# Optimization experiments

Hardware: AMD Instinct MI355X
Metric: run time of the kernel (lower is better)

The kernel has to match this reference:

```python
import jax, jax.numpy as jnp
import numpy as np

SCORE_THR = 0.005   # score_thres is None in init -> default 0.005
IOU_THR = 0.5
TOPK = 1024         # fixed pre-NMS candidate cap (JAX needs static shapes)


def setup_inputs() -> dict:
    key = jax.random.key(0)
    # (B, 4+nc, N_anchors): 16 images, 80 classes, 33600 anchors (1280x1280, strides 8/16/32)
    x = jax.random.normal(key, (16, 84, 33600), dtype=jnp.float32)
    return {"x": x}


def _pairwise_iou(b):
    # b: (K, 4) xyxy. Same math as torchvision.ops.box_iou.
    lt = jnp.maximum(b[:, None, :2], b[None, :, :2])   # (K, K, 2)
    rb = jnp.minimum(b[:, None, 2:], b[None, :, 2:])   # (K, K, 2)
    wh = jnp.clip(rb - lt, 0.0)
    inter = wh[..., 0] * wh[..., 1]
    area = (b[:, 2] - b[:, 0]) * (b[:, 3] - b[:, 1])
    union = area[:, None] + area[None, :] - inter
    return inter / jnp.maximum(union, 1e-9)


def _nms_single(boxes, svals, cids):
    # boxes (N,4); svals (N,) with -inf where score <= threshold; cids (N,) int
    top_s, idx = jax.lax.top_k(svals, TOPK)            # score-descending candidates
    b = boxes[idx]                                      # (K, 4)
    c = cids[idx]                                       # (K,)
    valid = top_s > SCORE_THR                           # thresholded-out slots are -inf
    iou = _pairwise_iou(b)                              # (K, K)
    ar = jnp.arange(TOPK)

    def body(i, keep):
        # greedy NMS: box i (if still kept) suppresses lower-scored boxes with IoU > thr
        sup = (iou[i] > IOU_THR) & (ar > i) & keep[i]
        return keep & ~sup

    keep = jax.lax.fori_loop(0, TOPK, body, valid)
    out = jnp.concatenate([b, top_s[:, None], c[:, None].astype(jnp.float32)], axis=1)  # (K, 6)
    out = jnp.where(keep[:, None], out, 0.0)            # padded fixed-size result
    return out, keep


def reference(x):
    xt = jnp.transpose(x, (0, 2, 1))                    # (B, N, 4+nc)
    boxes, scores = xt[..., :4], xt[..., 4:]
    svals = scores.max(-1)                              # (B, N)
    cids = scores.argmax(-1)                            # (B, N)
    svals = jnp.where(svals > SCORE_THR, svals, -jnp.inf)  # score-threshold mask
    out, keep = jax.vmap(_nms_single)(boxes, svals, cids)
    # out: (B, TOPK, 6) zero-padded [xyxy, score, cls]; keep: (B, TOPK) validity mask
    return out, keep
```

## Files before the change

### kernel.cpp

```cpp
#include <hip/hip_runtime.h>
#include <cstdint>
#include <cstddef>

#define NB 16
#define NC 84
#define NA 33600
#define NCLS 80
#define TOPK 1024
#define NBIN 8192
#define CANDCAP 8192
#define SELCAP 2048
#define SCORE_THR 0.005f
#define IOU_THR 0.5f
#define SBLK 33
#define SORTT 1024

__device__ __forceinline__ unsigned mono_u32(float f) {
    unsigned u = __float_as_uint(f);
    return (u & 0x80000000u) ? ~u : (u | 0x80000000u);
}
__device__ __forceinline__ float key_val(uint64_t k) {
    unsigned u = (unsigned)(k >> 32);
    u = (u & 0x80000000u) ? (u & 0x7FFFFFFFu) : ~u;
    return __uint_as_float(u);
}
__device__ __forceinline__ int key_idx(uint64_t k) {
    return (int)(~(uint32_t)(k & 0xFFFFFFFFu));
}

__global__ __launch_bounds__(256) void score_hist_kernel(const float* __restrict__ x,
                                                         float* __restrict__ sval,
                                                         int* __restrict__ cid,
                                                         unsigned* __restrict__ hist) {
    int b = blockIdx.x / SBLK;
    int blk = blockIdx.x - b * SBLK;
    int t = threadIdx.x;
    __shared__ unsigned h[NBIN];
    for (int i = t; i < NBIN; i += 256) h[i] = 0;
    __syncthreads();

    int q = blk * 256 + t;
    if (q < NA / 4) {
        const float4* p = (const float4*)(x + (size_t)b * NC * NA + (size_t)4 * NA) + q;
        float4 best = p[0];
        int4 bc = {0, 0, 0, 0};
#pragma unroll 4
        for (int c = 1; c < NCLS; ++c) {
            float4 v = p[(size_t)c * (NA / 4)];
            if (v.x > best.x) { best.x = v.x; bc.x = c; }
            if (v.y > best.y) { best.y = v.y; bc.y = c; }
            if (v.z > best.z) { best.z = v.z; bc.z = c; }
            if (v.w > best.w) { best.w = v.w; bc.w = c; }
        }
        float4 s;
        s.x = (best.x > SCORE_THR) ? best.x : -INFINITY;
        s.y = (best.y > SCORE_THR) ? best.y : -INFINITY;
        s.z = (best.z > SCORE_THR) ? best.z : -INFINITY;
        s.w = (best.w > SCORE_THR) ? best.w : -INFINITY;
        ((float4*)(sval + (size_t)b * NA))[q] = s;
        ((int4*)(cid + (size_t)b * NA))[q] = bc;
        atomicAdd(&h[mono_u32(s.x) >> 19], 1u);
        atomicAdd(&h[mono_u32(s.y) >> 19], 1u);
        atomicAdd(&h[mono_u32(s.z) >> 19], 1u);
        atomicAdd(&h[mono_u32(s.w) >> 19], 1u);
    }
    __syncthreads();
    unsigned* gh = hist + (size_t)b * NBIN;
    for (int i = t; i < NBIN; i += 256)
        if (h[i]) atomicAdd(&gh[i], h[i]);
}

__global__ __launch_bounds__(256) void scan_kernel(const unsigned* __restrict__ hist,
                                                   unsigned* __restrict__ cutbin) {
    int b = blockIdx.x;
    int t = threadIdx.x;
    __shared__ unsigned csum[256];
    const unsigned* h = hist + (size_t)b * NBIN;
    unsigned local = 0;
#pragma unroll 8
    for (int q = 0; q < 32; ++q) local += h[NBIN - 1 - (t * 32 + q)];
    csum[t] = local;
    __syncthreads();
    for (int off = 1; off < 256; off <<= 1) {
        unsigned v = (t >= off) ? csum[t - off] : 0u;
        __syncthreads();
        csum[t] += v;
        __syncthreads();
    }
    unsigned incl = csum[t], excl = incl - local;
    if (excl < TOPK && incl >= TOPK) {
        unsigned cum = excl;
        for (int q = 0; q < 32; ++q) {
            unsigned bin = NBIN - 1 - (t * 32 + q);
            unsigned c = h[bin];
            if (cum + c >= TOPK) { cutbin[b] = bin; break; }
            cum += c;
        }
    }
}

__global__ __launch_bounds__(256) void compact_kernel(const float* __restrict__ sval,
                                                      const unsigned* __restrict__ cutbin,
                                                      uint64_t* __restrict__ cand,
                                                      unsigned* __restrict__ cnt) {
    int gid = blockIdx.x * 256 + threadIdx.x;
    int b = gid / NA;
    int a = gid - b * NA;
    int b_first = (blockIdx.x * 256) / NA;
    int seg = b - b_first;
    __shared__ unsigned lcnt[2], lbase[2];
    __shared__ uint64_t k0[256], k1[256];
    if (threadIdx.x < 2) lcnt[threadIdx.x] = 0;
    __syncthreads();
    unsigned u = mono_u32(sval[gid]);
    if ((u >> 19) >= cutbin[b]) {
        unsigned pos = atomicAdd(&lcnt[seg], 1u);
        uint64_t key = ((uint64_t)u << 32) | (uint32_t)(~(uint32_t)a);
        if (seg) k1[pos] = key; else k0[pos] = key;
    }
    __syncthreads();
    if (threadIdx.x == 0 && lcnt[0]) lbase[0] = atomicAdd(&cnt[b_first * 64], lcnt[0]);
    if (threadIdx.x == 1 && lcnt[1]) lbase[1] = atomicAdd(&cnt[(b_first + 1) * 64], lcnt[1]);
    __syncthreads();
    if (threadIdx.x < lcnt[0]) {
        unsigned p = lbase[0] + threadIdx.x;
        if (p < CANDCAP) cand[((size_t)b_first << 13) + p] = k0[threadIdx.x];
    }
    if (threadIdx.x < lcnt[1]) {
        unsigned p = lbase[1] + threadIdx.x;
        if (p < CANDCAP) cand[((size_t)(b_first + 1) << 13) + p] = k1[threadIdx.x];
    }
}

__device__ __forceinline__ void bitonic_desc(uint64_t* A, int n, int tid, int T) {
    for (int k = 2; k <= n; k <<= 1) {
        for (int j = k >> 1; j > 0; j >>= 1) {
            for (int i = tid; i < n; i += T) {
                int ixj = i ^ j;
                if (ixj > i) {
                    uint64_t a = A[i], b2 = A[ixj];
                    bool up = ((i & k) == 0);
                    if (up ? (a < b2) : (a > b2)) { A[i] = b2; A[ixj] = a; }
                }
            }
            __syncthreads();
        }
    }
}

__global__ __launch_bounds__(SORTT) void sortk_kernel(const uint64_t* __restrict__ cand,
                                                      const unsigned* __restrict__ cnt,
                                                      const unsigned* __restrict__ cutbin,
                                                      const float* __restrict__ x,
                                                      const int* __restrict__ cid,
                                                      float* __restrict__ tval,
                                                      float* __restrict__ bx1, float* __restrict__ by1,
                                                      float* __restrict__ bx2, float* __restrict__ by2,
                                                      float* __restrict__ bar, int* __restrict__ tcid) {
    int b = blockIdx.x;
    int t = threadIdx.x;
    __shared__ uint64_t lk[CANDCAP];
    __shared__ uint64_t lsel[SELCAP];
    __shared__ unsigned sh[256];
    __shared__ unsigned snA, snSel, ssubcut;
    unsigned C = cnt[b * 64];
    if (C > CANDCAP) C = CANDCAP;
    unsigned cb = cutbin[b];

    for (int i = t; i < CANDCAP; i += SORTT)
        lk[i] = (i < (int)C) ? cand[((size_t)b << 13) + i] : 0ULL;
    for (int i = t; i < SELCAP; i += SORTT) lsel[i] = 0ULL;
    if (t < 256) sh[t] = 0;
    if (t == 0) { snA = 0; snSel = 0; }
    __syncthreads();

    unsigned myA = 0;
    for (int i = t; i < (int)C; i += SORTT) {
        unsigned u = (unsigned)(lk[i] >> 32);
        if ((u >> 19) > cb) myA++;
        else atomicAdd(&sh[(u >> 11) & 255u], 1u);
    }
    if (myA) atomicAdd(&snA, myA);
    __syncthreads();

    if (t == 0) {
        unsigned r = TOPK - snA;
        unsigned cum = 0, sc = 0;
        for (int s = 255; s >= 0; --s) {
            cum += sh[s];
            if (cum >= r) { sc = (unsigned)s; break; }
        }
        ssubcut = sc;
    }
    __syncthreads();
    unsigned subcut = ssubcut;

    int lane = t & 63;
    for (int i = t; i < (int)C; i += SORTT) {
        unsigned u = (unsigned)(lk[i] >> 32);
        unsigned bin = u >> 19;
        bool sel = (bin > cb) || (bin == cb && ((u >> 11) & 255u) >= subcut);
        uint64_t mask = __ballot(sel);
        if (mask) {
            int ldr = __ffsll((unsigned long long)mask) - 1;
            unsigned base = 0;
            if (lane == ldr) base = atomicAdd(&snSel, (unsigned)__popcll(mask));
            base = __shfl(base, ldr, 64);
            if (sel) {
                unsigned p = base + (unsigned)__popcll(mask & ((1ULL << lane) - 1ULL));
                if (p < SELCAP) lsel[p] = lk[i];
            }
        }
    }
    __syncthreads();
    unsigned nSel = snSel;

    uint64_t* buf;
    if (nSel <= SELCAP) { bitonic_desc(lsel, SELCAP, t, SORTT); buf = lsel; }
    else                { bitonic_desc(lk, CANDCAP, t, SORTT);  buf = lk;  }

    const float* xb = x + (size_t)b * NC * NA;
    const int* cidb = cid + (size_t)b * NA;
    int base_o = b << 10;
    for (int i = t; i < TOPK; i += SORTT) {
        uint64_t key = buf[i];
        tval[base_o + i] = key_val(key);
        int idx = key_idx(key);
        float X1 = xb[idx], Y1 = xb[NA + idx];
        float X2 = xb[2 * NA + idx], Y2 = xb[3 * NA + idx];
        bx1[base_o + i] = X1; by1[base_o + i] = Y1;
        bx2[base_o + i] = X2; by2[base_o + i] = Y2;
        bar[base_o + i] = (X2 - X1) * (Y2 - Y1);
        tcid[base_o + i] = cidb[idx];
    }
}

#define LDSPAD(j) ((j) + ((j) >> 6))
__global__ __launch_bounds__(256) void maskbuild_kernel(const float* __restrict__ bx1,
                                                        const float* __restrict__ by1,
                                                        const float* __restrict__ bx2,
                                                        const float* __restrict__ by2,
                                                        const float* __restrict__ bar,
                                                        const float* __restrict__ tval,
                                                        uint64_t* __restrict__ M,
                                                        int* __restrict__ rowflag) {
    int b = blockIdx.x >> 6;
    int r0 = (blockIdx.x & 63) << 4;
    int t = threadIdx.x;
    int r = r0 + (t & 15);
    int w = t >> 4;
    int base = b << 10;
    __shared__ float sx1[TOPK + 16], sy1[TOPK + 16], sx2[TOPK + 16], sy2[TOPK + 16], sar[TOPK + 16];
    __shared__ int anyf[256];

    for (int j = t; j < TOPK; j += 256) {
        int ji = LDSPAD(j);
        sx1[ji] = bx1[base + j]; sy1[ji] = by1[base + j];
        sx2[ji] = bx2[base + j]; sy2[ji] = by2[base + j];
        sar[ji] = bar[base + j];
    }
    __syncthreads();

    int ri = LDSPAD(r);
    float ix1 = sx1[ri], iy1 = sy1[ri], ix2 = sx2[ri], iy2 = sy2[ri], ia = sar[ri];
    uint64_t m = 0;
    if (((w << 6) + 63) > r) {
#pragma unroll 8
        for (int jj = 0; jj < 64; ++jj) {
            int j = (w << 6) + jj;
            int ji = w * 65 + jj;
            float ltx = fmaxf(ix1, sx1[ji]);
            float lty = fmaxf(iy1, sy1[ji]);
            float rbx = fminf(ix2, sx2[ji]);
            float rby = fminf(iy2, sy2[ji]);
            float ww = fmaxf(rbx - ltx, 0.0f);
            float hh = fmaxf(rby - lty, 0.0f);
            float inter = ww * hh;
            float uni = ia + sar[ji] - inter;
            float iou = inter / fmaxf(uni, 1e-9f);
            if (j > r && iou > IOU_THR) m |= (1ULL << jj);
        }
    }
    M[((size_t)(base + r) << 4) + w] = m;
    anyf[t] = (m != 0ULL);
    __syncthreads();
    if (t < 16) {
        int any = 0;
#pragma unroll
        for (int q = 0; q < 16; ++q) any |= anyf[(q << 4) + t];
        bool valid = tval[base + r0 + t] > SCORE_THR;
        rowflag[base + r0 + t] = (any && valid) ? 1 : 0;
    }
}

__global__ __launch_bounds__(64) void sweep_kernel(const uint64_t* __restrict__ M,
                                                   const int* __restrict__ rowflag,
                                                   const float* __restrict__ tval,
                                                   const int* __restrict__ tcid,
                                                   const float* __restrict__ bx1,
                                                   const float* __restrict__ by1,
                                                   const float* __restrict__ bx2,
                                                   const float* __restrict__ by2,
                                                   float* __restrict__ out) {
    int b = blockIdx.x;
    int l = threadIdx.x;
    int base = b << 10;
    int w = l & 15, g = l >> 4;
    __shared__ int list[TOPK];

    float tv[16];
#pragma unroll
    for (int s = 0; s < 16; ++s) tv[s] = tval[base + (s << 6) + l];

    uint64_t vword = 0;
#pragma unroll
    for (int s = 0; s < 16; ++s) {
        uint64_t bal = __ballot(tv[s] > SCORE_THR);
        if (l == s) vword = bal;
    }

    int cnt = 0;
#pragma unroll
    for (int s = 0; s < 16; ++s) {
        int flag = rowflag[base + (s << 6) + l];
        uint64_t m = __ballot(flag != 0);
        if (flag) {
            int pos = cnt + __popcll(m & ((1ULL << l) - 1ULL));
            list[pos] = (s << 6) + l;
        }
        cnt += __popcll(m);
    }
    __syncthreads();

    uint64_t remv = 0;
    for (int chunk = 0; chunk < cnt; chunk += 64) {
        int m = min(64, cnt - chunk);
        int idx_l = chunk + l;
        int myi = list[(idx_l < cnt) ? idx_l : 0];
        uint64_t rows[16];
#pragma unroll
        for (int q = 0; q < 16; ++q) {
            int it = chunk + q * 4 + g;
            int it2 = (it < cnt) ? it : 0;
            uint64_t v = M[((size_t)(base + list[it2]) << 4) + w];
            rows[q] = (it < cnt) ? v : 0ULL;
        }
        for (int r = 0; r < m; ++r) {
            int i = __shfl(myi, r, 64);
            uint64_t row = __shfl(rows[r >> 2], ((r & 3) << 4) + w, 64);
            uint64_t rb = __shfl(remv, i >> 6, 64);
            bool kept = !((rb >> (i & 63)) & 1ULL);
            remv |= (kept && l < 16) ? row : 0ULL;
        }
    }

    uint64_t kf = vword & ~remv;
#pragma unroll
    for (int s = 0; s < 16; ++s) {
        uint64_t kw = __shfl(kf, s, 64);
        bool kp = (kw >> l) & 1ULL;
        int k = (s << 6) + l;
        float x1 = bx1[base + k], y1 = by1[base + k];
        float x2 = bx2[base + k], y2 = by2[base + k];
        float* po = out + ((size_t)(base + k)) * 6;
        po[0] = kp ? x1 : 0.0f;
        po[1] = kp ? y1 : 0.0f;
        po[2] = kp ? x2 : 0.0f;
        po[3] = kp ? y2 : 0.0f;
        po[4] = kp ? tv[s] : 0.0f;
        po[5] = kp ? (float)tcid[base + k] : 0.0f;
        out[(size_t)NB * TOPK * 6 + base + k] = kp ? 1.0f : 0.0f;
    }
}

extern "C" void kernel_launch(void* const* d_in, const int* in_sizes, int n_in,
                              void* d_out, int out_size, void* d_ws, size_t ws_size,
                              hipStream_t stream) {
    const float* x = (const float*)d_in[0];
    float* out = (float*)d_out;
    char* ws = (char*)d_ws;

    size_t off = 0;
    auto alloc = [&](size_t bytes) { void* p = ws + off; off = (off + bytes + 255) & ~(size_t)255; return p; };
    float*    sval    = (float*)alloc((size_t)NB * NA * 4);
    int*      cid     = (int*)alloc((size_t)NB * NA * 4);
    unsigned* hist    = (unsigned*)alloc((size_t)NB * NBIN * 4);
    unsigned* cutbin  = (unsigned*)alloc(NB * 4);
    unsigned* cnt     = (unsigned*)alloc((size_t)NB * 64 * 4);
    uint64_t* cand    = (uint64_t*)alloc((size_t)NB * CANDCAP * 8);
    float*    tval    = (float*)alloc((size_t)NB * TOPK * 4);
    float*    bx1     = (float*)alloc((size_t)NB * TOPK * 4);
    float*    by1     = (float*)alloc((size_t)NB * TOPK * 4);
    float*    bx2     = (float*)alloc((size_t)NB * TOPK * 4);
    float*    by2     = (float*)alloc((size_t)NB * TOPK * 4);
    float*    bar     = (float*)alloc((size_t)NB * TOPK * 4);
    int*      tcid    = (int*)alloc((size_t)NB * TOPK * 4);
    int*      rowflag = (int*)alloc((size_t)NB * TOPK * 4);
    uint64_t* M       = (uint64_t*)alloc((size_t)NB * TOPK * 16 * 8);

    hipMemsetAsync(hist, 0, (size_t)NB * NBIN * 4, stream);
    hipMemsetAsync(cnt, 0, (size_t)NB * 64 * 4, stream);

    score_hist_kernel<<<NB * SBLK, 256, 0, stream>>>(x, sval, cid, hist);
    scan_kernel<<<NB, 256, 0, stream>>>(hist, cutbin);
    compact_kernel<<<NB * NA / 256, 256, 0, stream>>>(sval, cutbin, cand, cnt);
    sortk_kernel<<<NB, SORTT, 0, stream>>>(cand, cnt, cutbin, x, cid, tval, bx1, by1, bx2, by2, bar, tcid);
    maskbuild_kernel<<<NB * 64, 256, 0, stream>>>(bx1, by1, bx2, by2, bar, tval, M, rowflag);
    sweep_kernel<<<NB, 64, 0, stream>>>(M, rowflag, tval, tcid, bx1, by1, bx2, by2, out);
}
```

Before: 354.6 us.

## Replace bitonic top-k sort with parallel rank counting and batch mask rows

```diff
diff --git a/kernel.cpp b/kernel.cpp
--- a/kernel.cpp
+++ b/kernel.cpp
@@ -9,11 +9,10 @@
 #define TOPK 1024
 #define NBIN 8192
 #define CANDCAP 8192
-#define SELCAP 2048
 #define SCORE_THR 0.005f
 #define IOU_THR 0.5f
 #define SBLK 33
-#define SORTT 1024
+#define RBLK 8
 
 __device__ __forceinline__ unsigned mono_u32(float f) {
     unsigned u = __float_as_uint(f);
@@ -132,110 +131,54 @@
     }
 }
 
-__device__ __forceinline__ void bitonic_desc(uint64_t* A, int n, int tid, int T) {
-    for (int k = 2; k <= n; k <<= 1) {
-        for (int j = k >> 1; j > 0; j >>= 1) {
-            for (int i = tid; i < n; i += T) {
-                int ixj = i ^ j;
-                if (ixj > i) {
-                    uint64_t a = A[i], b2 = A[ixj];
-                    bool up = ((i & k) == 0);
-                    if (up ? (a < b2) : (a > b2)) { A[i] = b2; A[ixj] = a; }
-                }
-            }
-            __syncthreads();
-        }
-    }
-}
-
-__global__ __launch_bounds__(SORTT) void sortk_kernel(const uint64_t* __restrict__ cand,
-                                                      const unsigned* __restrict__ cnt,
-                                                      const unsigned* __restrict__ cutbin,
-                                                      const float* __restrict__ x,
-                                                      const int* __restrict__ cid,
-                                                      float* __restrict__ tval,
-                                                      float* __restrict__ bx1, float* __restrict__ by1,
-                                                      float* __restrict__ bx2, float* __restrict__ by2,
-                                                      float* __restrict__ bar, int* __restrict__ tcid) {
-    int b = blockIdx.x;
+__global__ __launch_bounds__(256) void rank_kernel(const uint64_t* __restrict__ cand,
+                                                   const unsigned* __restrict__ cnt,
+                                                   const float* __restrict__ x,
+                                                   const int* __restrict__ cid,
+                                                   float* __restrict__ tval,
+                                                   float* __restrict__ bx1, float* __restrict__ by1,
+                                                   float* __restrict__ bx2, float* __restrict__ by2,
+                                                   float* __restrict__ bar, int* __restrict__ tcid) {
+    int b = blockIdx.x / RBLK;
+    int sub = blockIdx.x - b * RBLK;
     int t = threadIdx.x;
-    __shared__ uint64_t lk[CANDCAP];
-    __shared__ uint64_t lsel[SELCAP];
-    __shared__ unsigned sh[256];
-    __shared__ unsigned snA, snSel, ssubcut;
+    __shared__ uint64_t keys[CANDCAP];
     unsigned C = cnt[b * 64];
     if (C > CANDCAP) C = CANDCAP;
-    unsigned cb = cutbin[b];
-
-    for (int i = t; i < CANDCAP; i += SORTT)
-        lk[i] = (i < (int)C) ? cand[((size_t)b << 13) + i] : 0ULL;
-    for (int i = t; i < SELCAP; i += SORTT) lsel[i] = 0ULL;
-    if (t < 256) sh[t] = 0;
-    if (t == 0) { snA = 0; snSel = 0; }
-    __syncthreads();
-
-    unsigned myA = 0;
-    for (int i = t; i < (int)C; i += SORTT) {
-        unsigned u = (unsigned)(lk[i] >> 32);
-        if ((u >> 19) > cb) myA++;
-        else atomicAdd(&sh[(u >> 11) & 255u], 1u);
-    }
-    if (myA) atomicAdd(&snA, myA);
-    __syncthreads();
-
-    if (t == 0) {
-        unsigned r = TOPK - snA;
-        unsigned cum = 0, sc = 0;
-        for (int s = 255; s >= 0; --s) {
-            cum += sh[s];
-            if (cum >= r) { sc = (unsigned)s; break; }
-        }
-        ssubcut = sc;
-    }
-    __syncthreads();
-    unsigned subcut = ssubcut;
-
-    int lane = t & 63;
-    for (int i = t; i < (int)C; i += SORTT) {
-        unsigned u = (unsigned)(lk[i] >> 32);
-        unsigned bin = u >> 19;
-        bool sel = (bin > cb) || (bin == cb && ((u >> 11) & 255u) >= subcut);
-        uint64_t mask = __ballot(sel);
-        if (mask) {
-            int ldr = __ffsll((unsigned long long)mask) - 1;
-            unsigned base = 0;
-            if (lane == ldr) base = atomicAdd(&snSel, (unsigned)__popcll(mask));
-            base = __shfl(base, ldr, 64);
-            if (sel) {
-                unsigned p = base + (unsigned)__popcll(mask & ((1ULL << lane) - 1ULL));
-                if (p < SELCAP) lsel[p] = lk[i];
-            }
-        }
-    }
-    __syncthreads();
-    unsigned nSel = snSel;
-
-    uint64_t* buf;
-    if (nSel <= SELCAP) { bitonic_desc(lsel, SELCAP, t, SORTT); buf = lsel; }
-    else                { bitonic_desc(lk, CANDCAP, t, SORTT);  buf = lk;  }
+    const uint64_t* cb = cand + ((size_t)b << 13);
+    for (int i = t; i < (int)C; i += 256) keys[i] = cb[i];
+    __syncthreads();
 
     const float* xb = x + (size_t)b * NC * NA;
     const int* cidb = cid + (size_t)b * NA;
     int base_o = b << 10;
-    for (int i = t; i < TOPK; i += SORTT) {
-        uint64_t key = buf[i];
-        tval[base_o + i] = key_val(key);
-        int idx = key_idx(key);
-        float X1 = xb[idx], Y1 = xb[NA + idx];
-        float X2 = xb[2 * NA + idx], Y2 = xb[3 * NA + idx];
-        bx1[base_o + i] = X1; by1[base_o + i] = Y1;
-        bx2[base_o + i] = X2; by2[base_o + i] = Y2;
-        bar[base_o + i] = (X2 - X1) * (Y2 - Y1);
-        tcid[base_o + i] = cidb[idx];
+    for (int p = sub * 256 + t; p < (int)C; p += RBLK * 256) {
+        uint64_t ki = keys[p];
+        unsigned rank = 0;
+        int j = 0;
+        for (; j + 4 <= (int)C; j += 4) {
+            rank += (keys[j]     > ki) ? 1u : 0u;
+            rank += (keys[j + 1] > ki) ? 1u : 0u;
+            rank += (keys[j + 2] > ki) ? 1u : 0u;
+            rank += (keys[j + 3] > ki) ? 1u : 0u;
+        }
+        for (; j < (int)C; ++j) rank += (keys[j] > ki) ? 1u : 0u;
+        if (rank < TOPK) {
+            int o = base_o + (int)rank;
+            tval[o] = key_val(ki);
+            int idx = key_idx(ki);
+            float X1 = xb[idx], Y1 = xb[NA + idx];
+            float X2 = xb[2 * NA + idx], Y2 = xb[3 * NA + idx];
+            bx1[o] = X1; by1[o] = Y1;
+            bx2[o] = X2; by2[o] = Y2;
+            bar[o] = (X2 - X1) * (Y2 - Y1);
+            tcid[o] = cidb[idx];
+        }
     }
 }
 
 #define LDSPAD(j) ((j) + ((j) >> 6))
+#define MBROWS 64
 __global__ __launch_bounds__(256) void maskbuild_kernel(const float* __restrict__ bx1,
                                                         const float* __restrict__ by1,
                                                         const float* __restrict__ bx2,
@@ -244,14 +187,14 @@
                                                         const float* __restrict__ tval,
                                                         uint64_t* __restrict__ M,
                                                         int* __restrict__ rowflag) {
-    int b = blockIdx.x >> 6;
-    int r0 = (blockIdx.x & 63) << 4;
+    int b = blockIdx.x >> 4;
+    int r0 = (blockIdx.x & 15) << 6;
     int t = threadIdx.x;
-    int r = r0 + (t & 15);
+    int rsub = t & 15;
     int w = t >> 4;
     int base = b << 10;
     __shared__ float sx1[TOPK + 16], sy1[TOPK + 16], sx2[TOPK + 16], sy2[TOPK + 16], sar[TOPK + 16];
-    __shared__ int anyf[256];
+    __shared__ unsigned aflag[MBROWS];
 
     for (int j = t; j < TOPK; j += 256) {
         int ji = LDSPAD(j);
@@ -259,37 +202,40 @@
         sx2[ji] = bx2[base + j]; sy2[ji] = by2[base + j];
         sar[ji] = bar[base + j];
     }
-    __syncthreads();
-
-    int ri = LDSPAD(r);
-    float ix1 = sx1[ri], iy1 = sy1[ri], ix2 = sx2[ri], iy2 = sy2[ri], ia = sar[ri];
-    uint64_t m = 0;
-    if (((w << 6) + 63) > r) {
+    if (t < MBROWS) aflag[t] = 0;
+    __syncthreads();
+
+#pragma unroll
+    for (int rr = 0; rr < 4; ++rr) {
+        int r = r0 + (rr << 4) + rsub;
+        int ri = LDSPAD(r);
+        float ix1 = sx1[ri], iy1 = sy1[ri], ix2 = sx2[ri], iy2 = sy2[ri], ia = sar[ri];
+        uint64_t m = 0;
+        if (((w << 6) + 63) > r) {
 #pragma unroll 8
-        for (int jj = 0; jj < 64; ++jj) {
-            int j = (w << 6) + jj;
-            int ji = w * 65 + jj;
-            float ltx = fmaxf(ix1, sx1[ji]);
-            float lty = fmaxf(iy1, sy1[ji]);
-            float rbx = fminf(ix2, sx2[ji]);
-            float rby = fminf(iy2, sy2[ji]);
-            float ww = fmaxf(rbx - ltx, 0.0f);
-            float hh = fmaxf(rby - lty, 0.0f);
-            float inter = ww * hh;
-            float uni = ia + sar[ji] - inter;
-            float iou = inter / fmaxf(uni, 1e-9f);
-            if (j > r && iou > IOU_THR) m |= (1ULL << jj);
-        }
-    }
-    M[((size_t)(base + r) << 4) + w] = m;
-    anyf[t] = (m != 0ULL);
-    __syncthreads();
-    if (t < 16) {
-        int any = 0;
-#pragma unroll
-        for (int q = 0; q < 16; ++q) any |= anyf[(q << 4) + t];
-        bool valid = tval[base + r0 + t] > SCORE_THR;
-        rowflag[base + r0 + t] = (any && valid) ? 1 : 0;
+            for (int jj = 0; jj < 64; ++jj) {
+                int j = (w << 6) + jj;
+                int ji = w * 65 + jj;
+                float ltx = fmaxf(ix1, sx1[ji]);
+                float lty = fmaxf(iy1, sy1[ji]);
+                float rbx = fminf(ix2, sx2[ji]);
+                float rby = fminf(iy2, sy2[ji]);
+                float ww = fmaxf(rbx - ltx, 0.0f);
+                float hh = fmaxf(rby - lty, 0.0f);
+                float inter = ww * hh;
+                float uni = ia + sar[ji] - inter;
+                float iou = inter / fmaxf(uni, 1e-9f);
+                if (j > r && iou > IOU_THR) m |= (1ULL << jj);
+            }
+        }
+        M[((size_t)(base + r) << 4) + w] = m;
+        if (m) atomicOr(&aflag[(rr << 4) + rsub], 1u);
+    }
+    __syncthreads();
+    if (t < MBROWS) {
+        int r = r0 + t;
+        bool valid = tval[base + r] > SCORE_THR;
+        rowflag[base + r] = (aflag[t] && valid) ? 1 : 0;
     }
 }
 
@@ -385,8 +331,8 @@
     float*    sval    = (float*)alloc((size_t)NB * NA * 4);
     int*      cid     = (int*)alloc((size_t)NB * NA * 4);
     unsigned* hist    = (unsigned*)alloc((size_t)NB * NBIN * 4);
+    unsigned* cnt     = (unsigned*)alloc((size_t)NB * 64 * 4);
     unsigned* cutbin  = (unsigned*)alloc(NB * 4);
-    unsigned* cnt     = (unsigned*)alloc((size_t)NB * 64 * 4);
     uint64_t* cand    = (uint64_t*)alloc((size_t)NB * CANDCAP * 8);
     float*    tval    = (float*)alloc((size_t)NB * TOPK * 4);
     float*    bx1     = (float*)alloc((size_t)NB * TOPK * 4);
@@ -398,13 +344,12 @@
     int*      rowflag = (int*)alloc((size_t)NB * TOPK * 4);
     uint64_t* M       = (uint64_t*)alloc((size_t)NB * TOPK * 16 * 8);
 
-    hipMemsetAsync(hist, 0, (size_t)NB * NBIN * 4, stream);
-    hipMemsetAsync(cnt, 0, (size_t)NB * 64 * 4, stream);
+    hipMemsetAsync(hist, 0, (size_t)NB * NBIN * 4 + (size_t)NB * 64 * 4, stream);
 
     score_hist_kernel<<<NB * SBLK, 256, 0, stream>>>(x, sval, cid, hist);
     scan_kernel<<<NB, 256, 0, stream>>>(hist, cutbin);
     compact_kernel<<<NB * NA / 256, 256, 0, stream>>>(sval, cutbin, cand, cnt);
-    sortk_kernel<<<NB, SORTT, 0, stream>>>(cand, cnt, cutbin, x, cid, tval, bx1, by1, bx2, by2, bar, tcid);
-    maskbuild_kernel<<<NB * 64, 256, 0, stream>>>(bx1, by1, bx2, by2, bar, tval, M, rowflag);
+    rank_kernel<<<NB * RBLK, 256, 0, stream>>>(cand, cnt, x, cid, tval, bx1, by1, bx2, by2, bar, tcid);
+    maskbuild_kernel<<<NB * 16, 256, 0, stream>>>(bx1, by1, bx2, by2, bar, tval, M, rowflag);
     sweep_kernel<<<NB, 64, 0, stream>>>(M, rowflag, tval, tcid, bx1, by1, bx2, by2, out);
 }
```

New measurement: 348.9 us (median of 2 runs). About the same (-1.6%).
